# Optimization experiments

Measured on AMD Instinct MI355X. Metric: run time of the kernel, lower is better.

The kernel has to match this reference:

```python
import jax, jax.numpy as jnp
import numpy as np

IN_DIM = 768
OUT_DIM = 4096
N_SK_ITER = 3
TARGET_TEMP = 0.06
PRED_TEMP = 0.12
PREFACTOR = 1.0
EXP_MAX = 50.0  # exp_max_values[float32]
SK_EPS = 1e-8
NORM_EPS = 1e-7


def setup_inputs() -> dict:
    key = jax.random.key(0)
    kx, kw = jax.random.split(key)
    x = jax.random.normal(kx, (16, 1024, IN_DIM), dtype=jnp.float32)
    # nn.Linear weight init: normal(std=1); bias zeros
    weight = jax.random.normal(kw, (OUT_DIM, IN_DIM), dtype=jnp.float32)
    bias = jnp.zeros((OUT_DIM,), dtype=jnp.float32)
    return {"x": x, "weight": weight, "bias": bias}


def sinkhorn_knopp(M, n_iterations, eps=SK_EPS):
    # stable_exp: shift by max over dim=-2 (token axis), add EXP_MAX
    shift = jnp.max(M, axis=-2, keepdims=True)
    M = jnp.exp(M + EXP_MAX - shift)
    for _ in range(n_iterations):  # small fixed count
        M = M / (jnp.sum(M, axis=-2, keepdims=True) + eps)  # column normalize
        M = M / (jnp.sum(M, axis=-1, keepdims=True) + eps)  # row normalize
    return M


def reference(x, weight, bias):
    # L2 normalize features (eps matches torch F.normalize with p=2)
    norm = jnp.maximum(jnp.linalg.norm(x, axis=-1, keepdims=True), NORM_EPS)
    x_n = x / norm
    logits = jnp.einsum("bnd,kd->bnk", x_n, weight) + bias  # [B, N, K]
    # positionwise_sk=True: no flatten before sinkhorn; detach -> stop_gradient
    assignments = sinkhorn_knopp(jax.lax.stop_gradient(logits) / TARGET_TEMP, N_SK_ITER)
    tgt = assignments.reshape(-1, OUT_DIM).astype(jnp.float32)
    pred = logits.reshape(-1, OUT_DIM).astype(jnp.float32)
    loss = -jnp.mean(jnp.sum(tgt * jax.nn.log_softmax(pred / PRED_TEMP, axis=-1), axis=-1))
    return assignments, PREFACTOR * loss
```

## Files before the change

kernel.cpp:

```cpp
#include <hip/hip_runtime.h>
#include <math.h>

#define BATCH 16
#define NTOK  1024
#define NCLU  4096
#define DIM   768
#define MROWS (BATCH * NTOK)

constexpr float TT_INV    = 16.666666666666668f;
constexpr float PT_INV    = 8.333333333333334f;
constexpr float SK_EPS_   = 1e-8f;
constexpr float NORM_EPS_ = 1e-7f;
constexpr float COL_SHIFT = 60.0f;
constexpr float P_SHIFT   = 40.0f;

typedef _Float16 f16x8 __attribute__((ext_vector_type(8)));
typedef _Float16 f16x4 __attribute__((ext_vector_type(4)));
typedef float    f32x4 __attribute__((ext_vector_type(4)));

struct F8 { float v[8]; };

__device__ __forceinline__ F8 load8(const float* p) {
    const float4 a = *(const float4*)p;
    const float4 b = *(const float4*)(p + 4);
    return F8{{a.x, a.y, a.z, a.w, b.x, b.y, b.z, b.w}};
}
__device__ __forceinline__ F8 load8(const _Float16* p) {
    f16x8 h = *(const f16x8*)p;
    F8 r;
#pragma unroll
    for (int i = 0; i < 8; ++i) r.v[i] = (float)h[i];
    return r;
}

__device__ __forceinline__ float wave_sum(float s) {
#pragma unroll
    for (int off = 32; off; off >>= 1) s += __shfl_xor(s, off);
    return s;
}

__device__ __forceinline__ void gl_lds16(const void* g, void* l) {
    __builtin_amdgcn_global_load_lds(
        (const __attribute__((address_space(1))) unsigned int*)g,
        (__attribute__((address_space(3))) unsigned int*)l,
        16, 0, 0);
}

__global__ __launch_bounds__(256) void castx_kernel(
    const float* __restrict__ x, _Float16* __restrict__ x16)
{
    int row  = (blockIdx.x * 256 + threadIdx.x) >> 6;
    int lane = threadIdx.x & 63;
    const float4* rp = (const float4*)(x + (size_t)row * DIM);
    float4 v[3];
    float ss = 0.f;
#pragma unroll
    for (int i = 0; i < 3; ++i) {
        v[i] = rp[lane + i * 64];
        ss += v[i].x * v[i].x + v[i].y * v[i].y + v[i].z * v[i].z + v[i].w * v[i].w;
    }
    ss = wave_sum(ss);
    float sc = 1.0f / fmaxf(sqrtf(ss), NORM_EPS_);
    _Float16* op = x16 + (size_t)row * DIM;
#pragma unroll
    for (int i = 0; i < 3; ++i) {
        f16x4 h;
        h[0] = (_Float16)(v[i].x * sc); h[1] = (_Float16)(v[i].y * sc);
        h[2] = (_Float16)(v[i].z * sc); h[3] = (_Float16)(v[i].w * sc);
        *(f16x4*)(op + 4 * (lane + i * 64)) = h;
    }
}

__global__ __launch_bounds__(256) void castw_kernel(
    const float* __restrict__ w, _Float16* __restrict__ w16)
{
    int i = blockIdx.x * 256 + threadIdx.x;
    const float4 a = *(const float4*)(w + (size_t)i * 8);
    const float4 b = *(const float4*)(w + (size_t)i * 8 + 4);
    f16x8 h;
    h[0] = (_Float16)a.x; h[1] = (_Float16)a.y; h[2] = (_Float16)a.z; h[3] = (_Float16)a.w;
    h[4] = (_Float16)b.x; h[5] = (_Float16)b.y; h[6] = (_Float16)b.z; h[7] = (_Float16)b.w;
    *(f16x8*)(w16 + (size_t)i * 8) = h;
}

__global__ __launch_bounds__(256) void rownorm_kernel(
    const float* __restrict__ x, float* __restrict__ invn)
{
    int wave = (blockIdx.x * 256 + threadIdx.x) >> 6;
    int lane = threadIdx.x & 63;
    const float4* row = (const float4*)(x + (size_t)wave * DIM);
    float s = 0.f;
#pragma unroll
    for (int i = 0; i < 3; ++i) {
        float4 v = row[lane + i * 64];
        s += v.x * v.x + v.y * v.y + v.z * v.z + v.w * v.w;
    }
    s = wave_sum(s);
    if (lane == 0) invn[wave] = 1.0f / fmaxf(sqrtf(s), NORM_EPS_);
}

#define BM 128
#define BN 128
#define BK 32

__global__ __launch_bounds__(256) void gemm16(
    const _Float16* __restrict__ A,
    const _Float16* __restrict__ B,
    const float* __restrict__ bias,
    _Float16* __restrict__ out,
    float* __restrict__ colpart)
{
    __shared__ __align__(16) _Float16 As[2][BM * BK];
    __shared__ __align__(16) _Float16 Bs[2][BN * BK];

    const int tid  = threadIdx.x;
    const int lane = tid & 63;
    const int wid  = tid >> 6;
    const int wr = wid >> 1, wc = wid & 1;

    const int nwg = gridDim.x;
    const int cpx = nwg >> 3;
    const int bid = blockIdx.x;
    const int swz = (bid & 7) * cpx + (bid >> 3);
    const int brow = (swz >> 5) * BM;
    const int bcol = (swz & 31) * BN;

    const int r  = lane >> 2;
    const int s4 = lane & 3;
    const int srcslot = s4 ^ (r & 3) ^ (r >> 2);
    const int c0 = wid * 2, c1 = wid * 2 + 1;

    const _Float16* gA0 = A + (size_t)(brow + c0 * 16 + r) * DIM + srcslot * 8;
    const _Float16* gA1 = A + (size_t)(brow + c1 * 16 + r) * DIM + srcslot * 8;
    const _Float16* gB0 = B + (size_t)(bcol + c0 * 16 + r) * DIM + srcslot * 8;
    const _Float16* gB1 = B + (size_t)(bcol + c1 * 16 + r) * DIM + srcslot * 8;
    const int oA0 = c0 * 16 * BK, oA1 = c1 * 16 * BK;

    const int q  = lane >> 4;
    const int fr = lane & 15;
    const int slot = q ^ (fr & 3) ^ ((fr >> 2) & 3);
    const int aoff = (wr * 64 + fr) * BK + slot * 8;
    const int boff = (wc * 64 + fr) * BK + slot * 8;

    f32x4 acc[4][4] = {};

    gl_lds16(gA0, &As[0][oA0]);
    gl_lds16(gA1, &As[0][oA1]);
    gl_lds16(gB0, &Bs[0][oA0]);
    gl_lds16(gB1, &Bs[0][oA1]);

    const int NT = DIM / BK;
    for (int kt = 0; kt < NT; ++kt) {
        const int cur = kt & 1;
        if (kt + 1 < NT) {
            const int nxt = cur ^ 1;
            const int ko = (kt + 1) * BK;
            gl_lds16(gA0 + ko, &As[nxt][oA0]);
            gl_lds16(gA1 + ko, &As[nxt][oA1]);
            gl_lds16(gB0 + ko, &Bs[nxt][oA0]);
            gl_lds16(gB1 + ko, &Bs[nxt][oA1]);
            asm volatile("s_waitcnt vmcnt(4)" ::: "memory");
        } else {
            asm volatile("s_waitcnt vmcnt(0)" ::: "memory");
        }
        __builtin_amdgcn_sched_barrier(0);
        __builtin_amdgcn_s_barrier();
        asm volatile("" ::: "memory");

        f16x8 af[4], bf[4];
#pragma unroll
        for (int m = 0; m < 4; ++m)
            af[m] = *(const f16x8*)&As[cur][aoff + m * 16 * BK];
#pragma unroll
        for (int n = 0; n < 4; ++n)
            bf[n] = *(const f16x8*)&Bs[cur][boff + n * 16 * BK];
        asm volatile("s_waitcnt lgkmcnt(0)" ::: "memory");
        __builtin_amdgcn_sched_barrier(0);
        __builtin_amdgcn_s_barrier();

#pragma unroll
        for (int m = 0; m < 4; ++m)
#pragma unroll
            for (int n = 0; n < 4; ++n)
                acc[m][n] = __builtin_amdgcn_mfma_f32_16x16x32_f16(
                    af[m], bf[n], acc[m][n], 0, 0, 0);
    }

    __syncthreads();
    float* cred = (float*)&As[0][0];

#pragma unroll
    for (int n = 0; n < 4; ++n) {
        int col = bcol + wc * 64 + n * 16 + fr;
        float bv = bias[col];
        float cs = 0.f;
#pragma unroll
        for (int m = 0; m < 4; ++m) {
            int row0 = brow + wr * 64 + m * 16 + (q << 2);
#pragma unroll
            for (int j = 0; j < 4; ++j) {
                float v = acc[m][n][j] + bv;
                out[(size_t)(row0 + j) * NCLU + col] = (_Float16)v;
                cs += __expf(v * TT_INV - COL_SHIFT);
            }
        }
        cs += __shfl_xor(cs, 16);
        cs += __shfl_xor(cs, 32);
        if (q == 0) cred[((wr * 2 + wc) * 4 + n) * 16 + fr] = cs;
    }
    __syncthreads();
    if (tid < 128) {
        int wc2 = tid >> 6, n2 = (tid >> 4) & 3, fr2 = tid & 15;
        float S = cred[((0 * 2 + wc2) * 4 + n2) * 16 + fr2]
                + cred[((1 * 2 + wc2) * 4 + n2) * 16 + fr2];
        colpart[(size_t)(brow >> 7) * NCLU + bcol + wc2 * 64 + n2 * 16 + fr2] = S;
    }
}

__global__ __launch_bounds__(256) void colfin_kernel(
    const float* __restrict__ part, float* __restrict__ a1)
{
    int i = blockIdx.x * 256 + threadIdx.x;
    int b = i >> 12, k = i & (NCLU - 1);
    const float* p = part + (size_t)(b * 8) * NCLU + k;
    float s = 0.f;
#pragma unroll
    for (int rb = 0; rb < 8; ++rb) { s += *p; p += NCLU; }
    a1[i] = -COL_SHIFT - __logf(s);
}

#define LDK 40

__device__ __forceinline__ f16x8 pack8(float4 lo, float4 hi, float sc) {
    f16x8 h;
    h[0] = (_Float16)(lo.x * sc); h[1] = (_Float16)(lo.y * sc);
    h[2] = (_Float16)(lo.z * sc); h[3] = (_Float16)(lo.w * sc);
    h[4] = (_Float16)(hi.x * sc); h[5] = (_Float16)(hi.y * sc);
    h[6] = (_Float16)(hi.z * sc); h[7] = (_Float16)(hi.w * sc);
    return h;
}

template <typename OT>
__global__ __launch_bounds__(256) void gemm_f16(
    const float* __restrict__ x, const float* __restrict__ w,
    const float* __restrict__ bias, const float* __restrict__ invn,
    OT* __restrict__ out)
{
    __shared__ __align__(16) _Float16 As[BM * LDK];
    __shared__ __align__(16) _Float16 Bs[BN * LDK];

    const int tid  = threadIdx.x;
    const int lane = tid & 63;
    const int wid  = tid >> 6;
    const int wr = wid >> 1, wc = wid & 1;
    const int brow = blockIdx.y * BM;
    const int bcol = blockIdx.x * BN;

    const int r0 = tid >> 2;
    const int r1 = r0 + 64;
    const int kc = (tid & 3) * 8;
    const float sA0 = invn[brow + r0];
    const float sA1 = invn[brow + r1];
    const float* gA0 = x + (size_t)(brow + r0) * DIM + kc;
    const float* gA1 = x + (size_t)(brow + r1) * DIM + kc;
    const float* gB0 = w + (size_t)(bcol + r0) * DIM + kc;
    const float* gB1 = w + (size_t)(bcol + r1) * DIM + kc;

    f32x4 acc[4][4] = {};
    float4 a00, a01, a10, a11, b00, b01, b10, b11;
    a00 = *(const float4*)(gA0);     a01 = *(const float4*)(gA0 + 4);
    a10 = *(const float4*)(gA1);     a11 = *(const float4*)(gA1 + 4);
    b00 = *(const float4*)(gB0);     b01 = *(const float4*)(gB0 + 4);
    b10 = *(const float4*)(gB1);     b11 = *(const float4*)(gB1 + 4);

    const int NT = DIM / BK;
    for (int kt = 0; kt < NT; ++kt) {
        __syncthreads();
        *(f16x8*)&As[r0 * LDK + kc] = pack8(a00, a01, sA0);
        *(f16x8*)&As[r1 * LDK + kc] = pack8(a10, a11, sA1);
        *(f16x8*)&Bs[r0 * LDK + kc] = pack8(b00, b01, 1.0f);
        *(f16x8*)&Bs[r1 * LDK + kc] = pack8(b10, b11, 1.0f);
        __syncthreads();

        if (kt + 1 < NT) {
            int k0 = (kt + 1) * BK;
            a00 = *(const float4*)(gA0 + k0); a01 = *(const float4*)(gA0 + k0 + 4);
            a10 = *(const float4*)(gA1 + k0); a11 = *(const float4*)(gA1 + k0 + 4);
            b00 = *(const float4*)(gB0 + k0); b01 = *(const float4*)(gB0 + k0 + 4);
            b10 = *(const float4*)(gB1 + k0); b11 = *(const float4*)(gB1 + k0 + 4);
        }

        const int ko = (lane >> 4) * 8;
        f16x8 af[4], bf[4];
#pragma unroll
        for (int m = 0; m < 4; ++m)
            af[m] = *(const f16x8*)&As[(wr * 64 + m * 16 + (lane & 15)) * LDK + ko];
#pragma unroll
        for (int n = 0; n < 4; ++n)
            bf[n] = *(const f16x8*)&Bs[(wc * 64 + n * 16 + (lane & 15)) * LDK + ko];
#pragma unroll
        for (int m = 0; m < 4; ++m)
#pragma unroll
            for (int n = 0; n < 4; ++n)
                acc[m][n] = __builtin_amdgcn_mfma_f32_16x16x32_f16(
                    af[m], bf[n], acc[m][n], 0, 0, 0);
    }

#pragma unroll
    for (int n = 0; n < 4; ++n) {
        int col = bcol + wc * 64 + n * 16 + (lane & 15);
        float bv = bias[col];
#pragma unroll
        for (int m = 0; m < 4; ++m) {
            int row0 = brow + wr * 64 + m * 16 + ((lane >> 4) << 2);
#pragma unroll
            for (int j = 0; j < 4; ++j)
                out[(size_t)(row0 + j) * NCLU + col] = (OT)(acc[m][n][j] + bv);
        }
    }
}

template <typename T>
__global__ __launch_bounds__(256) void colpass_kernel(
    const T* __restrict__ L, const float* __restrict__ a_in,
    const float* __restrict__ b_in, float* __restrict__ a_out)
{
    __shared__ float bsh[NTOK];
    __shared__ float ss[4][64];
    int b = blockIdx.x >> 6;
    int k = ((blockIdx.x & 63) << 6) + (threadIdx.x & 63);
    int wv = threadIdx.x >> 6;
    int lane = threadIdx.x & 63;
    const bool first = (b_in == nullptr);
    if (first) {
        for (int i = threadIdx.x; i < NTOK; i += 256) bsh[i] = 0.f;
    } else {
        for (int i = threadIdx.x; i < NTOK; i += 256) bsh[i] = b_in[b * NTOK + i];
    }
    __syncthreads();
    float aval = first ? -COL_SHIFT : a_in[b * NCLU + k];
    const T* p = L + (size_t)b * NTOK * NCLU + (size_t)(wv * 256) * NCLU + k;
    float s = 0.f;
#pragma unroll 4
    for (int n = 0; n < 256; ++n) {
        s += __expf((float)(*p) * TT_INV + aval + bsh[wv * 256 + n]);
        p += NCLU;
    }
    ss[wv][lane] = s;
    __syncthreads();
    if (wv == 0) {
        float S = ss[0][lane] + ss[1][lane] + ss[2][lane] + ss[3][lane];
        a_out[b * NCLU + k] = aval - __logf(first ? S : S + SK_EPS_);
    }
}

template <typename T>
__global__ __launch_bounds__(256) void colpassV_kernel(
    const T* __restrict__ L, const float* __restrict__ a_in,
    const float* __restrict__ b_in, float* __restrict__ a_out)
{
    __shared__ float bsh[NTOK];
    __shared__ float red[16][16][8];
    const int b     = blockIdx.x >> 5;
    const int strip = blockIdx.x & 31;
    const int cc    = threadIdx.x & 15;
    const int rg    = threadIdx.x >> 4;
    const int col0  = strip * 128 + cc * 8;
    for (int i = threadIdx.x; i < NTOK; i += 256) bsh[i] = b_in[b * NTOK + i];
    __syncthreads();
    const float4 av0 = *(const float4*)(a_in + b * NCLU + col0);
    const float4 av1 = *(const float4*)(a_in + b * NCLU + col0 + 4);
    const float av[8] = {av0.x, av0.y, av0.z, av0.w, av1.x, av1.y, av1.z, av1.w};
    float s[8] = {};
    const T* p = L + (size_t)b * NTOK * NCLU + (size_t)rg * NCLU + col0;
    for (int it = 0; it < 64; ++it) {
        F8 Lv = load8(p);
        float bpv = bsh[it * 16 + rg];
#pragma unroll
        for (int j = 0; j < 8; ++j) s[j] += __expf(Lv.v[j] * TT_INV + av[j] + bpv);
        p += (size_t)16 * NCLU;
    }
#pragma unroll
    for (int j = 0; j < 8; ++j) red[rg][cc][j] = s[j];
    __syncthreads();
    if (threadIdx.x < 128) {
        int c2 = threadIdx.x >> 3, j2 = threadIdx.x & 7;
        float S = 0.f;
#pragma unroll
        for (int g = 0; g < 16; ++g) S += red[g][c2][j2];
        int col = strip * 128 + c2 * 8 + j2;
        a_out[b * NCLU + col] = a_in[b * NCLU + col] - __logf(S + SK_EPS_);
    }
}

template <typename T>
__global__ __launch_bounds__(256) void rowpass_kernel(
    const T* __restrict__ L, const float* __restrict__ a_in,
    const float* __restrict__ b_in, float* __restrict__ b_out)
{
    int row  = (blockIdx.x * 256 + threadIdx.x) >> 6;
    int lane = threadIdx.x & 63;
    int b = row >> 10;
    const T* Lr = L + (size_t)row * NCLU;
    const float* av = a_in + (size_t)b * NCLU;
    float bp = b_in ? b_in[row] : 0.f;
    float s = 0.f;
#pragma unroll
    for (int i = 0; i < 8; ++i) {
        int c = i * 64 + lane;
        F8 Lv = load8(Lr + c * 8);
        F8 Av = load8(av + c * 8);
#pragma unroll
        for (int j = 0; j < 8; ++j)
            s += __expf(Lv.v[j] * TT_INV + Av.v[j] + bp);
    }
    s = wave_sum(s);
    if (lane == 0) b_out[row] = bp - __logf(s + SK_EPS_);
}

template <typename T>
__global__ __launch_bounds__(256) void final_kernel(
    const T* __restrict__ L, const float* __restrict__ a3,
    const float* __restrict__ b2, float* __restrict__ out,
    float* __restrict__ rowloss)
{
    __shared__ float red[3][4];
    const int row  = blockIdx.x;
    const int tid  = threadIdx.x;
    const int lane = tid & 63;
    const int wv   = tid >> 6;
    const int b    = row >> 10;
    const T* Lr = L + (size_t)row * NCLU;
    const float* av = a3 + (size_t)b * NCLU;
    const float bp = b2[row];

    float e[2][8];
    float rs = 0.f, q = 0.f, sP = 0.f;
#pragma unroll
    for (int jj = 0; jj < 2; ++jj) {
        int c = tid + jj * 256;
        F8 Lv = load8(Lr + c * 8);
        F8 Av = load8(av + c * 8);
#pragma unroll
        for (int j = 0; j < 8; ++j) {
            float P  = Lv.v[j] * PT_INV;
            float ev = __expf(Lv.v[j] * TT_INV + Av.v[j] + bp);
            e[jj][j] = ev;
            rs += ev;
            q  += ev * P;
            sP += __expf(P - P_SHIFT);
        }
    }
    rs = wave_sum(rs); q = wave_sum(q); sP = wave_sum(sP);
    if (lane == 0) { red[0][wv] = rs; red[1][wv] = q; red[2][wv] = sP; }
    __syncthreads();
    rs = red[0][0] + red[0][1] + red[0][2] + red[0][3];
    q  = red[1][0] + red[1][1] + red[1][2] + red[1][3];
    sP = red[2][0] + red[2][1] + red[2][2] + red[2][3];

    const float inv = 1.0f / (rs + SK_EPS_);
    const float lse = P_SHIFT + __logf(sP);

    float* Or = out + (size_t)row * NCLU;
#pragma unroll
    for (int jj = 0; jj < 2; ++jj) {
        int c = tid + jj * 256;
        f32x4 w0, w1;
        w0[0] = e[jj][0] * inv; w0[1] = e[jj][1] * inv;
        w0[2] = e[jj][2] * inv; w0[3] = e[jj][3] * inv;
        w1[0] = e[jj][4] * inv; w1[1] = e[jj][5] * inv;
        w1[2] = e[jj][6] * inv; w1[3] = e[jj][7] * inv;
        __builtin_nontemporal_store(w0, (f32x4*)(Or + c * 8));
        __builtin_nontemporal_store(w1, (f32x4*)(Or + c * 8 + 4));
    }
    if (tid == 0) rowloss[row] = q * inv - lse * (rs * inv);
}

__global__ __launch_bounds__(256) void lossred_kernel(
    const float* __restrict__ rowloss, float* __restrict__ out_loss)
{
    __shared__ float red[4];
    int tid = threadIdx.x, lane = tid & 63, wv = tid >> 6;
    float s = 0.f;
    for (int i = tid; i < MROWS; i += 256) s += rowloss[i];
    s = wave_sum(s);
    if (lane == 0) red[wv] = s;
    __syncthreads();
    if (tid == 0)
        out_loss[0] = -(red[0] + red[1] + red[2] + red[3]) / (float)MROWS;
}

extern "C" void kernel_launch(void* const* d_in, const int* in_sizes, int n_in,
                              void* d_out, int out_size, void* d_ws, size_t ws_size,
                              hipStream_t stream)
{
    const float* x    = (const float*)d_in[0];
    const float* w    = (const float*)d_in[1];
    const float* bias = (const float*)d_in[2];
    float* out = (float*)d_out;
    char* base = (char*)d_ws;
    float* ws  = (float*)d_ws;

    float* a1      = ws;
    float* a2      = a1 + BATCH * NCLU;
    float* a3      = a2 + BATCH * NCLU;
    float* b1      = a3 + BATCH * NCLU;
    float* b2      = b1 + MROWS;
    float* rowloss = b2 + MROWS;

    const size_t SMALL = 1u << 20;
    const size_t L16B  = (size_t)MROWS * NCLU * 2;
    const size_t X16B  = (size_t)MROWS * DIM * 2;
    const size_t W16B  = (size_t)NCLU * DIM * 2;
    const size_t PARTB = (size_t)128 * NCLU * 4;

    const int CB = BATCH * (NCLU / 64);
    const int RB = MROWS / 4;

    if (ws_size >= SMALL + L16B + X16B + W16B + PARTB) {
        _Float16* L16 = (_Float16*)(base + SMALL);
        _Float16* X16 = (_Float16*)(base + SMALL + L16B);
        _Float16* W16 = (_Float16*)(base + SMALL + L16B + X16B);
        float*    part = (float*)(base + SMALL + L16B + X16B + W16B);
        castx_kernel<<<MROWS / 4, 256, 0, stream>>>(x, X16);
        castw_kernel<<<(NCLU * DIM / 8) / 256, 256, 0, stream>>>(w, W16);
        gemm16<<<(MROWS / BM) * (NCLU / BN), 256, 0, stream>>>(X16, W16, bias, L16, part);
        colfin_kernel<<<BATCH * NCLU / 256, 256, 0, stream>>>(part, a1);
        rowpass_kernel<_Float16><<<RB, 256, 0, stream>>>(L16, a1, nullptr, b1);
        colpassV_kernel<_Float16><<<BATCH * 32, 256, 0, stream>>>(L16, a1, b1, a2);
        rowpass_kernel<_Float16><<<RB, 256, 0, stream>>>(L16, a2, b1, b2);
        colpassV_kernel<_Float16><<<BATCH * 32, 256, 0, stream>>>(L16, a2, b2, a3);
        final_kernel<_Float16><<<MROWS, 256, 0, stream>>>(L16, a3, b2, out, rowloss);
        lossred_kernel<<<1, 256, 0, stream>>>(rowloss, out + (size_t)MROWS * NCLU);
    } else if (ws_size >= SMALL + L16B) {
        float* invn = rowloss + MROWS;
        _Float16* L16 = (_Float16*)(base + SMALL);
        rownorm_kernel<<<MROWS / 4, 256, 0, stream>>>(x, invn);
        dim3 gg(NCLU / BN, MROWS / BM);
        gemm_f16<_Float16><<<gg, 256, 0, stream>>>(x, w, bias, invn, L16);
        colpass_kernel<_Float16><<<CB, 256, 0, stream>>>(L16, nullptr, nullptr, a1);
        rowpass_kernel<_Float16><<<RB, 256, 0, stream>>>(L16, a1, nullptr, b1);
        colpassV_kernel<_Float16><<<BATCH * 32, 256, 0, stream>>>(L16, a1, b1, a2);
        rowpass_kernel<_Float16><<<RB, 256, 0, stream>>>(L16, a2, b1, b2);
        colpassV_kernel<_Float16><<<BATCH * 32, 256, 0, stream>>>(L16, a2, b2, a3);
        final_kernel<_Float16><<<MROWS, 256, 0, stream>>>(L16, a3, b2, out, rowloss);
        lossred_kernel<<<1, 256, 0, stream>>>(rowloss, out + (size_t)MROWS * NCLU);
    } else {
        float* invn = rowloss + MROWS;
        rownorm_kernel<<<MROWS / 4, 256, 0, stream>>>(x, invn);
        dim3 gg(NCLU / BN, MROWS / BM);
        gemm_f16<float><<<gg, 256, 0, stream>>>(x, w, bias, invn, out);
        colpass_kernel<float><<<CB, 256, 0, stream>>>(out, nullptr, nullptr, a1);
        rowpass_kernel<float><<<RB, 256, 0, stream>>>(out, a1, nullptr, b1);
        colpassV_kernel<float><<<BATCH * 32, 256, 0, stream>>>(out, a1, b1, a2);
        rowpass_kernel<float><<<RB, 256, 0, stream>>>(out, a2, b1, b2);
        colpassV_kernel<float><<<BATCH * 32, 256, 0, stream>>>(out, a2, b2, a3);
        final_kernel<float><<<MROWS, 256, 0, stream>>>(out, a3, b2, out, rowloss);
        lossred_kernel<<<1, 256, 0, stream>>>(rowloss, out + (size_t)MROWS * NCLU);
    }
}
```

Baseline: 367.9 us.

## Stage GEMM epilogue through LDS for coalesced stores; single-buffer K loop

The GEMM epilogue now writes the fp16 output tile into shared memory in two half-tile passes, then emits 16-byte vector stores per row, replacing scattered 2-byte global stores. To fit this into a smaller LDS footprint, the K loop drops double buffering and uses a single buffer with syncthreads before and after each direct-to-LDS load. This removes the overlap of global loads with MFMA compute, so each K step waits for its own load latency, while the output stores become coalesced.

```diff
diff --git a/kernel.cpp b/kernel.cpp
--- a/kernel.cpp
+++ b/kernel.cpp
@@ -110,8 +110,9 @@
     _Float16* __restrict__ out,
     float* __restrict__ colpart)
 {
-    __shared__ __align__(16) _Float16 As[2][BM * BK];
-    __shared__ __align__(16) _Float16 Bs[2][BN * BK];
+    __shared__ __align__(16) _Float16 sh[2 * BM * BK];
+    _Float16* As = sh;
+    _Float16* Bs = sh + BM * BK;
 
     const int tid  = threadIdx.x;
     const int lane = tid & 63;
@@ -134,7 +135,10 @@
     const _Float16* gA1 = A + (size_t)(brow + c1 * 16 + r) * DIM + srcslot * 8;
     const _Float16* gB0 = B + (size_t)(bcol + c0 * 16 + r) * DIM + srcslot * 8;
     const _Float16* gB1 = B + (size_t)(bcol + c1 * 16 + r) * DIM + srcslot * 8;
-    const int oA0 = c0 * 16 * BK, oA1 = c1 * 16 * BK;
+    _Float16* lA0 = &As[c0 * 16 * BK];
+    _Float16* lA1 = &As[c1 * 16 * BK];
+    _Float16* lB0 = &Bs[c0 * 16 * BK];
+    _Float16* lB1 = &Bs[c1 * 16 * BK];
 
     const int q  = lane >> 4;
     const int fr = lane & 15;
@@ -144,40 +148,23 @@
 
     f32x4 acc[4][4] = {};
 
-    gl_lds16(gA0, &As[0][oA0]);
-    gl_lds16(gA1, &As[0][oA1]);
-    gl_lds16(gB0, &Bs[0][oA0]);
-    gl_lds16(gB1, &Bs[0][oA1]);
-
     const int NT = DIM / BK;
     for (int kt = 0; kt < NT; ++kt) {
-        const int cur = kt & 1;
-        if (kt + 1 < NT) {
-            const int nxt = cur ^ 1;
-            const int ko = (kt + 1) * BK;
-            gl_lds16(gA0 + ko, &As[nxt][oA0]);
-            gl_lds16(gA1 + ko, &As[nxt][oA1]);
-            gl_lds16(gB0 + ko, &Bs[nxt][oA0]);
-            gl_lds16(gB1 + ko, &Bs[nxt][oA1]);
-            asm volatile("s_waitcnt vmcnt(4)" ::: "memory");
-        } else {
-            asm volatile("s_waitcnt vmcnt(0)" ::: "memory");
-        }
-        __builtin_amdgcn_sched_barrier(0);
-        __builtin_amdgcn_s_barrier();
-        asm volatile("" ::: "memory");
+        const int ko = kt * BK;
+        __syncthreads();
+        gl_lds16(gA0 + ko, lA0);
+        gl_lds16(gA1 + ko, lA1);
+        gl_lds16(gB0 + ko, lB0);
+        gl_lds16(gB1 + ko, lB1);
+        __syncthreads();
 
         f16x8 af[4], bf[4];
 #pragma unroll
         for (int m = 0; m < 4; ++m)
-            af[m] = *(const f16x8*)&As[cur][aoff + m * 16 * BK];
+            af[m] = *(const f16x8*)&As[aoff + m * 16 * BK];
 #pragma unroll
         for (int n = 0; n < 4; ++n)
-            bf[n] = *(const f16x8*)&Bs[cur][boff + n * 16 * BK];
-        asm volatile("s_waitcnt lgkmcnt(0)" ::: "memory");
-        __builtin_amdgcn_sched_barrier(0);
-        __builtin_amdgcn_s_barrier();
-
+            bf[n] = *(const f16x8*)&Bs[boff + n * 16 * BK];
 #pragma unroll
         for (int m = 0; m < 4; ++m)
 #pragma unroll
@@ -186,27 +173,46 @@
                     af[m], bf[n], acc[m][n], 0, 0, 0);
     }
 
-    __syncthreads();
-    float* cred = (float*)&As[0][0];
-
-#pragma unroll
-    for (int n = 0; n < 4; ++n) {
-        int col = bcol + wc * 64 + n * 16 + fr;
-        float bv = bias[col];
-        float cs = 0.f;
-#pragma unroll
-        for (int m = 0; m < 4; ++m) {
-            int row0 = brow + wr * 64 + m * 16 + (q << 2);
-#pragma unroll
-            for (int j = 0; j < 4; ++j) {
-                float v = acc[m][n][j] + bv;
-                out[(size_t)(row0 + j) * NCLU + col] = (_Float16)v;
-                cs += __expf(v * TT_INV - COL_SHIFT);
+    float cs[4] = {0.f, 0.f, 0.f, 0.f};
+    _Float16* Ct = sh;
+#pragma unroll
+    for (int h = 0; h < 2; ++h) {
+        __syncthreads();
+        if (wr == h) {
+#pragma unroll
+            for (int n = 0; n < 4; ++n) {
+                const int coll = wc * 64 + n * 16 + fr;
+                const float bv = bias[bcol + coll];
+#pragma unroll
+                for (int m = 0; m < 4; ++m) {
+#pragma unroll
+                    for (int j = 0; j < 4; ++j) {
+                        float v = acc[m][n][j] + bv;
+                        Ct[(m * 16 + (q << 2) + j) * BN + coll] = (_Float16)v;
+                        cs[n] += __expf(v * TT_INV - COL_SHIFT);
+                    }
+                }
             }
         }
-        cs += __shfl_xor(cs, 16);
-        cs += __shfl_xor(cs, 32);
-        if (q == 0) cred[((wr * 2 + wc) * 4 + n) * 16 + fr] = cs;
+        __syncthreads();
+#pragma unroll
+        for (int i = 0; i < 4; ++i) {
+            int c   = tid + i * 256;
+            int rl  = c >> 4;
+            int c16 = c & 15;
+            f16x8 v = *(const f16x8*)&Ct[rl * BN + c16 * 8];
+            *(f16x8*)(out + (size_t)(brow + h * 64 + rl) * NCLU + bcol + c16 * 8) = v;
+        }
+    }
+
+    __syncthreads();
+    float* cred = (float*)sh;
+#pragma unroll
+    for (int n = 0; n < 4; ++n) {
+        float c2 = cs[n];
+        c2 += __shfl_xor(c2, 16);
+        c2 += __shfl_xor(c2, 32);
+        if (q == 0) cred[((wr * 2 + wc) * 4 + n) * 16 + fr] = c2;
     }
     __syncthreads();
     if (tid < 128) {
```

Measured after the change: 375.8 us. +2.1%, slower.
